# Kernel tuning notes

Measured on AMD Instinct MI355X. Metric: run time of the kernel, lower is better.

Reference implementation:

```python
import jax, jax.numpy as jnp
import numpy as np
from jax import lax

# ---- module config (matches init_kwargs) ----
TARGET_H, TARGET_W = 1024, 1024
SMOOTH_K = 3
DIL_K = 3
DIL_ITERS = 2
DIL_BETA = 5.0
DIL_STRENGTH = 1.0


def _cubic_weights(t):
    """Keys cubic convolution weights (a=-0.75, torch bicubic). t: [N] frac in [0,1). -> [N,4] for taps at offsets -1,0,1,2."""
    a = -0.75
    t1 = t + 1.0  # distance of tap -1
    w0 = a * t1**3 - 5.0 * a * t1**2 + 8.0 * a * t1 - 4.0 * a
    w1 = (a + 2.0) * t**3 - (a + 3.0) * t**2 + 1.0
    u = 1.0 - t
    w2 = (a + 2.0) * u**3 - (a + 3.0) * u**2 + 1.0
    u2 = 2.0 - t
    w3 = a * u2**3 - 5.0 * a * u2**2 + 8.0 * a * u2 - 4.0 * a
    return jnp.stack([w0, w1, w2, w3], axis=-1)


def _taps(n_in, n_out):
    # grid_sample with align_corners=True over a full linspace(-1,1) grid maps
    # output pixel j -> input coord linspace(0, n_in-1, n_out)[j]
    src = jnp.linspace(0.0, n_in - 1.0, n_out)
    i0 = jnp.floor(src)
    t = src - i0
    idx = (i0[:, None] + jnp.arange(-1, 3)[None, :]).astype(jnp.int32)
    idx = jnp.clip(idx, 0, n_in - 1)  # padding_mode='border'
    return idx, _cubic_weights(t)


def _resize_bicubic(x, ht, wt):
    B, C, H, W = x.shape
    ih, wh = _taps(H, ht)
    iw, ww = _taps(W, wt)
    # rows: [B,C,ht,4,W] -> weighted sum over taps
    xr = x[:, :, ih, :]
    xr = jnp.einsum('bcthw,th->bctw', xr.transpose(0, 1, 2, 4, 3), wh) if False else (xr * wh[None, None, :, :, None]).sum(axis=3)
    # cols: [B,C,ht,wt,4]
    xc = xr[:, :, :, iw]
    return (xc * ww[None, None, None, :, :]).sum(axis=-1)


def _gaussian_kernel(k):
    sigma = k / 3.0
    r = np.arange(k, dtype=np.float32) - k // 2
    k1 = np.exp(-0.5 * (r / sigma) ** 2)
    k1 = k1 / k1.sum()
    k2 = np.outer(k1, k1)
    return jnp.asarray(k2.reshape(1, 1, k, k))


def _smooth(x):
    kern = _gaussian_kernel(SMOOTH_K)
    pad = SMOOTH_K // 2
    return lax.conv_general_dilated(
        x, kern, window_strides=(1, 1), padding=[(pad, pad), (pad, pad)],
        dimension_numbers=('NCHW', 'OIHW', 'NCHW'))


def _soft_dilate(x):
    # windowed logsumexp: lse = (1/beta) * log sum_window exp(beta * x),
    # with zero padding inside the window (matches F.unfold padding).
    p = DIL_K // 2
    for _ in range(DIL_ITERS):
        xp = jnp.pad(x, ((0, 0), (0, 0), (p, p), (p, p)))
        e = jnp.exp(DIL_BETA * (xp - 1.0))  # shift by 1.0 (x in [0,1]) for stability
        s = lax.reduce_window(e, 0.0, lax.add, (1, 1, DIL_K, DIL_K), (1, 1, 1, 1), 'VALID')
        x = jnp.clip(1.0 + jnp.log(s) / DIL_BETA, 0.0, 1.0)
    return x  # DIL_STRENGTH == 1.0 -> no blend with original


def setup_inputs() -> dict:
    key = jax.random.key(0)
    detris_output = jax.random.normal(key, (8, 1, 256, 256), dtype=jnp.float32)
    return {"detris_output": detris_output}


def reference(detris_output) -> jnp.ndarray:
    x = jax.nn.sigmoid(detris_output)
    x = _resize_bicubic(x, TARGET_H, TARGET_W)
    x = _smooth(x)
    x = _soft_dilate(x)
    return x
```

## Files before the change

kernel.cpp:

```cpp
#include <hip/hip_runtime.h>
#include <hip/hip_fp16.h>

#define B_ 8
#define HI 256
#define WI 256
#define HO 1024
#define WO 1024

#define TLE 64
#define NRS 24
#define SSTR 25
#define HS 18
#define EW 38
#define SC (255.0f / 1023.0f)
#define F5L2E 7.2134752f
#define EXPM5 0.0067379470f
#define GW0 0.27406862f
#define GW1 0.45186276f
#define C02 0.13862944f

__device__ __forceinline__ int basef(int g) {
    int yc = min(max(g, 0), HO - 1);
    return (int)floorf((float)yc * SC) - 2;
}

__device__ __forceinline__ void tap6(int g, int* base_out, float w[6]) {
    int yc = min(max(g, 0), HO - 1);
    int base = basef(g);
#pragma unroll
    for (int s = 0; s < 6; ++s) w[s] = 0.0f;
    if (g >= 0 && g < HO) {
#pragma unroll
        for (int d = -1; d <= 1; ++d) {
            int yd = yc + d;
            if (yd < 0 || yd >= HO) continue;
            float src = (float)yd * SC;
            float fi0 = floorf(src);
            float tt = src - fi0;
            const float a = -0.75f;
            float t1 = tt + 1.0f;
            float c0 = ((a * t1 - 5.0f * a) * t1 + 8.0f * a) * t1 - 4.0f * a;
            float c1 = ((a + 2.0f) * tt - (a + 3.0f)) * tt * tt + 1.0f;
            float u = 1.0f - tt;
            float c2 = ((a + 2.0f) * u - (a + 3.0f)) * u * u + 1.0f;
            float u2 = 2.0f - tt;
            float c3 = ((a * u2 - 5.0f * a) * u2 + 8.0f * a) * u2 - 4.0f * a;
            int s0 = ((int)fi0 - 1) - base;
            float gg = (d == 0) ? GW1 : GW0;
            w[s0 + 0] += gg * c0;
            w[s0 + 1] += gg * c1;
            w[s0 + 2] += gg * c2;
            w[s0 + 3] += gg * c3;
        }
    }
    *base_out = base;
}

__device__ __forceinline__ void pad8(const float w[6], int d, float scl, float w8[8]) {
#pragma unroll
    for (int j = 0; j < 8; ++j) {
        float a = (j < 6) ? w[j] : 0.0f;
        float bq = (j >= 1 && j < 7) ? w[j - 1] : 0.0f;
        w8[j] = ((d == 0) ? a : bq) * scl;
    }
}

__device__ __forceinline__ uint4 packw8(const float w8[8]) {
    uint4 r;
    r.x = __builtin_bit_cast(unsigned int, __floats2half2_rn(w8[0], w8[1]));
    r.y = __builtin_bit_cast(unsigned int, __floats2half2_rn(w8[2], w8[3]));
    r.z = __builtin_bit_cast(unsigned int, __floats2half2_rn(w8[4], w8[5]));
    r.w = __builtin_bit_cast(unsigned int, __floats2half2_rn(w8[6], w8[7]));
    return r;
}

__device__ __forceinline__ void unpackw8(uint4 p, float w[8]) {
    __half2 a = __builtin_bit_cast(__half2, p.x);
    __half2 bq = __builtin_bit_cast(__half2, p.y);
    __half2 c = __builtin_bit_cast(__half2, p.z);
    __half2 d = __builtin_bit_cast(__half2, p.w);
    w[0] = __low2float(a);  w[1] = __high2float(a);
    w[2] = __low2float(bq); w[3] = __high2float(bq);
    w[4] = __low2float(c);  w[5] = __high2float(c);
    w[6] = __low2float(d);  w[7] = __high2float(d);
}

__global__ __launch_bounds__(256, 8) void k_fused(const float* __restrict__ in,
                                                  float* __restrict__ out) {
    __shared__ __align__(16) unsigned int Eu[68 * EW];
    __shared__ float4 Hs[NRS * HS];
    __shared__ uint4 xWu[72];
    __shared__ uint4 vWu[70];
    __shared__ int vgb[14], xgb[18];
    float* SL = (float*)Eu;

    const int tid = threadIdx.x;
    const int bx = blockIdx.x, by = blockIdx.y, b = blockIdx.z;
    const int gy0 = by * TLE, gx0 = bx * TLE;
    const int rlo = basef(gy0 - 3);
    const int clo = basef(gx0 - 4);

    if (tid < 70) {
        int fy = tid + 1;
        int base; float w[6];
        tap6(gy0 + fy - 3, &base, w);
        int q = tid / 5;
        int bs = basef(gy0 + (1 + 5 * q) - 3);
        float w8[8];
        pad8(w, base - bs, F5L2E, w8);
        vWu[tid] = packw8(w8);
    } else if (tid < 84) {
        vgb[tid - 70] = basef(gy0 + (1 + 5 * (tid - 70)) - 3);
    } else if (tid < 102) {
        xgb[tid - 84] = basef(gx0 + 4 * (tid - 84) - 4);
    } else if (tid >= 128 && tid < 200) {
        int xe = tid - 128;
        int base; float w[6];
        tap6(gx0 + xe - 4, &base, w);
        int bs = basef(gx0 + (xe & ~3) - 4);
        float w8[8];
        pad8(w, base - bs, 1.0f, w8);
        xWu[xe] = packw8(w8);
    }
    {
        const float* pin = in + b * (HI * WI);
        int cc = tid & 31, rr0 = tid >> 5;
        if (cc < NRS) {
            for (int rr = rr0; rr < NRS; rr += 8) {
                int row = min(max(rlo + rr, 0), HI - 1);
                int col = min(max(clo + cc, 0), HI - 1);
                float x = pin[row * WI + col];
                SL[rr * SSTR + cc] = 1.0f / (1.0f + __expf(-x));
            }
        }
    }
    __syncthreads();

    const int ty = tid / HS;
    const int tx = tid - ty * HS;

    if (tid < 252) {
        int cbg = xgb[tx] - clo;
        int wc[8];
#pragma unroll
        for (int j = 0; j < 8; ++j) wc[j] = min(cbg + j, NRS - 1);
        float xw0[8], xw1[8], xw2[8], xw3[8];
        {
            int xe0 = tx << 2;
            unpackw8(xWu[xe0 + 0], xw0);
            unpackw8(xWu[xe0 + 1], xw1);
            unpackw8(xWu[xe0 + 2], xw2);
            unpackw8(xWu[xe0 + 3], xw3);
        }
        for (int r = ty; r < NRS; r += 14) {
            const float* srow = SL + r * SSTR;
            float wnd[8];
#pragma unroll
            for (int j = 0; j < 8; ++j) wnd[j] = srow[wc[j]];
            float s0 = wnd[0]*xw0[0], s1 = wnd[0]*xw1[0], s2 = wnd[0]*xw2[0], s3 = wnd[0]*xw3[0];
#pragma unroll
            for (int j = 1; j < 8; ++j) {
                s0 = fmaf(wnd[j], xw0[j], s0);
                s1 = fmaf(wnd[j], xw1[j], s1);
                s2 = fmaf(wnd[j], xw2[j], s2);
                s3 = fmaf(wnd[j], xw3[j], s3);
            }
            Hs[r * HS + tx] = make_float4(s0, s1, s2, s3);
        }
    }
    __syncthreads();

    if (tid < 252) {
        const int q = ty;
        const int rbase = vgb[q] - rlo;
        float4 h[8];
#pragma unroll
        for (int i = 0; i < 8; ++i) h[i] = Hs[min(rbase + i, NRS - 1) * HS + tx];
#pragma unroll
        for (int i = 0; i < 5; ++i) {
            int fy = 1 + 5 * q + i;
            if (fy <= 68) {
                float wv[8];
                unpackw8(vWu[fy - 1], wv);
                float ax = -F5L2E, ay = -F5L2E, az = -F5L2E, aw = -F5L2E;
#pragma unroll
                for (int j = 0; j < 8; ++j) {
                    ax = fmaf(wv[j], h[j].x, ax);
                    ay = fmaf(wv[j], h[j].y, ay);
                    az = fmaf(wv[j], h[j].z, az);
                    aw = fmaf(wv[j], h[j].w, aw);
                }
                unsigned int p0 = __builtin_bit_cast(unsigned int, __floats2half2_rn(exp2f(ax), exp2f(ay)));
                unsigned int p1 = __builtin_bit_cast(unsigned int, __floats2half2_rn(exp2f(az), exp2f(aw)));
                *reinterpret_cast<uint2*>(&Eu[(fy - 1) * EW + 2 * tx]) = make_uint2(p0, p1);
            }
        }
    }
    __syncthreads();

    {
        const int dx = tid & 15;
        const int sq = tid >> 4;
        const int lr0 = 4 * sq;
        const bool rT = (by == 0)  && (sq == 0);
        const bool rB = (by == 15) && (sq == 15);
        const bool cL = (bx == 0)  && (dx == 0);
        const bool cR = (bx == 15) && (dx == 15);

        auto HSUM = [&](int lr, float hs[6]) {
            unsigned int ua = Eu[lr * EW + 2 * dx + 1];
            uint2 ub = *reinterpret_cast<const uint2*>(&Eu[lr * EW + 2 * dx + 2]);
            unsigned int uc = Eu[lr * EW + 2 * dx + 4];
            __half2 A2 = __builtin_bit_cast(__half2, ua);
            __half2 B2 = __builtin_bit_cast(__half2, ub.x);
            __half2 C2 = __builtin_bit_cast(__half2, ub.y);
            __half2 D2 = __builtin_bit_cast(__half2, uc);
            float e0 = __low2float(A2), e1 = __high2float(A2);
            float e2 = __low2float(B2), e3 = __high2float(B2);
            float e4 = __low2float(C2), e5 = __high2float(C2);
            float e6 = __low2float(D2), e7 = __high2float(D2);
            hs[0] = e0 + e1 + e2;
            hs[1] = e1 + e2 + e3;
            hs[2] = e2 + e3 + e4;
            hs[3] = e3 + e4 + e5;
            hs[4] = e4 + e5 + e6;
            hs[5] = e5 + e6 + e7;
        };
        auto E2F = [&](const float* a, const float* bq, const float* c, bool rowOv) -> float4 {
            float e[6];
#pragma unroll
            for (int j = 0; j < 6; ++j) e[j] = fminf(a[j] + bq[j] + c[j], 1.0f);
            if (rowOv) {
#pragma unroll
                for (int j = 0; j < 6; ++j) e[j] = EXPM5;
            }
            if (cL) e[0] = EXPM5;
            if (cR) e[5] = EXPM5;
            return make_float4(e[0] + e[1] + e[2], e[1] + e[2] + e[3],
                               e[2] + e[3] + e[4], e[3] + e[4] + e[5]);
        };
        auto OUTF = [&](float4 a, float4 bq, float4 c) -> float4 {
            float4 o;
            o.x = fmaxf(fminf(fmaf(C02, __log2f(a.x + bq.x + c.x), 1.0f), 1.0f), 0.0f);
            o.y = fmaxf(fminf(fmaf(C02, __log2f(a.y + bq.y + c.y), 1.0f), 1.0f), 0.0f);
            o.z = fmaxf(fminf(fmaf(C02, __log2f(a.z + bq.z + c.z), 1.0f), 1.0f), 0.0f);
            o.w = fmaxf(fminf(fmaf(C02, __log2f(a.w + bq.w + c.w), 1.0f), 1.0f), 0.0f);
            return o;
        };

        float hA[6], hB[6], hC[6], hD[6];
        size_t obase = ((size_t)(b * HO + by * TLE + 4 * sq) * WO) + bx * TLE + (dx << 2);

        HSUM(lr0 + 0, hA); HSUM(lr0 + 1, hB); HSUM(lr0 + 2, hC);
        float4 eA = E2F(hA, hB, hC, rT);
        HSUM(lr0 + 3, hD); float4 eB = E2F(hB, hC, hD, false);
        HSUM(lr0 + 4, hA); float4 eC = E2F(hC, hD, hA, false);
        *reinterpret_cast<float4*>(out + obase) = OUTF(eA, eB, eC); obase += WO;
        HSUM(lr0 + 5, hB); float4 eD = E2F(hD, hA, hB, false);
        *reinterpret_cast<float4*>(out + obase) = OUTF(eB, eC, eD); obase += WO;
        HSUM(lr0 + 6, hC); float4 eE = E2F(hA, hB, hC, false);
        *reinterpret_cast<float4*>(out + obase) = OUTF(eC, eD, eE); obase += WO;
        HSUM(lr0 + 7, hD); float4 eF = E2F(hB, hC, hD, rB);
        *reinterpret_cast<float4*>(out + obase) = OUTF(eD, eE, eF);
    }
}

extern "C" void kernel_launch(void* const* d_in, const int* in_sizes, int n_in,
                              void* d_out, int out_size, void* d_ws, size_t ws_size,
                              hipStream_t stream) {
    const float* in = (const float*)d_in[0];
    float* out = (float*)d_out;
    dim3 g(WO / TLE, HO / TLE, B_);
    k_fused<<<g, dim3(256), 0, stream>>>(in, out);
}
```

Measured before the change: 24.96 us.

## Give each wavefront its own 32x32 tile to drop block-wide barriers

Restructures the fused kernel so each 64-lane wavefront processes an independent 32x32 output tile with private LDS buffers. This removes all __syncthreads between the sigmoid load, horizontal and vertical bicubic passes, and the dilation stage. The intermediate horizontal-pass results are also stored as fp16 instead of fp32 to cut LDS footprint. The smaller tiles recompute more halo per output and lower fp16 precision in the intermediate, and occupancy hint drops to 7.

```diff
diff --git a/kernel.cpp b/kernel.cpp
--- a/kernel.cpp
+++ b/kernel.cpp
@@ -1,23 +1,18 @@
 #include <hip/hip_runtime.h>
 #include <hip/hip_fp16.h>
 
-#define B_ 8
 #define HI 256
 #define WI 256
 #define HO 1024
 #define WO 1024
-
-#define TLE 64
-#define NRS 24
-#define SSTR 25
-#define HS 18
-#define EW 38
 #define SC (255.0f / 1023.0f)
 #define F5L2E 7.2134752f
 #define EXPM5 0.0067379470f
 #define GW0 0.27406862f
 #define GW1 0.45186276f
 #define C02 0.13862944f
+#define EST 22
+#define SLS 19
 
 __device__ __forceinline__ int basef(int g) {
     int yc = min(max(g, 0), HO - 1);
@@ -59,9 +54,10 @@
 __device__ __forceinline__ void pad8(const float w[6], int d, float scl, float w8[8]) {
 #pragma unroll
     for (int j = 0; j < 8; ++j) {
-        float a = (j < 6) ? w[j] : 0.0f;
-        float bq = (j >= 1 && j < 7) ? w[j - 1] : 0.0f;
-        w8[j] = ((d == 0) ? a : bq) * scl;
+        float v0 = (j < 6) ? w[j] : 0.0f;
+        float v1 = (j >= 1 && j < 7) ? w[j - 1] : 0.0f;
+        float v2 = (j >= 2) ? w[j - 2] : 0.0f;
+        w8[j] = ((d == 0) ? v0 : (d == 1) ? v1 : v2) * scl;
     }
 }
 
@@ -76,88 +72,87 @@
 
 __device__ __forceinline__ void unpackw8(uint4 p, float w[8]) {
     __half2 a = __builtin_bit_cast(__half2, p.x);
-    __half2 bq = __builtin_bit_cast(__half2, p.y);
+    __half2 b = __builtin_bit_cast(__half2, p.y);
     __half2 c = __builtin_bit_cast(__half2, p.z);
     __half2 d = __builtin_bit_cast(__half2, p.w);
     w[0] = __low2float(a);  w[1] = __high2float(a);
-    w[2] = __low2float(bq); w[3] = __high2float(bq);
+    w[2] = __low2float(b);  w[3] = __high2float(b);
     w[4] = __low2float(c);  w[5] = __high2float(c);
     w[6] = __low2float(d);  w[7] = __high2float(d);
 }
 
-__global__ __launch_bounds__(256, 8) void k_fused(const float* __restrict__ in,
+__device__ __forceinline__ void unpack4(uint2 u, float f[4]) {
+    __half2 a = __builtin_bit_cast(__half2, u.x);
+    __half2 b = __builtin_bit_cast(__half2, u.y);
+    f[0] = __low2float(a); f[1] = __high2float(a);
+    f[2] = __low2float(b); f[3] = __high2float(b);
+}
+
+__global__ __launch_bounds__(256, 7) void k_fused(const float* __restrict__ in,
                                                   float* __restrict__ out) {
-    __shared__ __align__(16) unsigned int Eu[68 * EW];
-    __shared__ float4 Hs[NRS * HS];
-    __shared__ uint4 xWu[72];
-    __shared__ uint4 vWu[70];
-    __shared__ int vgb[14], xgb[18];
-    float* SL = (float*)Eu;
+    __shared__ __align__(16) unsigned int Eu[4][36 * EST];
+    __shared__ __align__(16) unsigned int Hu[4][16 * EST];
+    __shared__ uint4 xWu[4][40];
+    __shared__ uint4 vWu[4][36];
 
     const int tid = threadIdx.x;
-    const int bx = blockIdx.x, by = blockIdx.y, b = blockIdx.z;
-    const int gy0 = by * TLE, gx0 = bx * TLE;
-    const int rlo = basef(gy0 - 3);
-    const int clo = basef(gx0 - 4);
-
-    if (tid < 70) {
-        int fy = tid + 1;
-        int base; float w[6];
-        tap6(gy0 + fy - 3, &base, w);
-        int q = tid / 5;
-        int bs = basef(gy0 + (1 + 5 * q) - 3);
+    const int w = tid >> 6, lane = tid & 63;
+    unsigned int* E1 = Eu[w];
+    unsigned int* Hq = Hu[w];
+    uint4* xW = xWu[w];
+    uint4* vW = vWu[w];
+    float* SL = (float*)E1;
+
+    const int tx = (blockIdx.x << 2) + w, ty = blockIdx.y, b = blockIdx.z;
+    const int gx0 = tx << 5, gy0 = ty << 5;
+    const int rlo = basef(gy0 - 2);
+    const int clo = basef(gx0 - 3);
+
+    if (lane < 36) {
+        int base; float w6[6];
+        tap6(gy0 + (lane + 1) - 3, &base, w6);
+        int bs = basef(gy0 + 6 * (lane / 6) - 2);
         float w8[8];
-        pad8(w, base - bs, F5L2E, w8);
-        vWu[tid] = packw8(w8);
-    } else if (tid < 84) {
-        vgb[tid - 70] = basef(gy0 + (1 + 5 * (tid - 70)) - 3);
-    } else if (tid < 102) {
-        xgb[tid - 84] = basef(gx0 + 4 * (tid - 84) - 4);
-    } else if (tid >= 128 && tid < 200) {
-        int xe = tid - 128;
-        int base; float w[6];
-        tap6(gx0 + xe - 4, &base, w);
-        int bs = basef(gx0 + (xe & ~3) - 4);
+        pad8(w6, base - bs, F5L2E, w8);
+        vW[lane] = packw8(w8);
+    }
+    if (lane < 40) {
+        int base; float w6[6];
+        tap6(gx0 + lane - 3, &base, w6);
+        int bs = basef(gx0 + 4 * (lane >> 2) - 3);
         float w8[8];
-        pad8(w, base - bs, 1.0f, w8);
-        xWu[xe] = packw8(w8);
+        pad8(w6, base - bs, 1.0f, w8);
+        xW[lane] = packw8(w8);
     }
     {
         const float* pin = in + b * (HI * WI);
-        int cc = tid & 31, rr0 = tid >> 5;
-        if (cc < NRS) {
-            for (int rr = rr0; rr < NRS; rr += 8) {
-                int row = min(max(rlo + rr, 0), HI - 1);
-                int col = min(max(clo + cc, 0), HI - 1);
-                float x = pin[row * WI + col];
-                SL[rr * SSTR + cc] = 1.0f / (1.0f + __expf(-x));
-            }
-        }
-    }
-    __syncthreads();
-
-    const int ty = tid / HS;
-    const int tx = tid - ty * HS;
-
-    if (tid < 252) {
-        int cbg = xgb[tx] - clo;
-        int wc[8];
-#pragma unroll
-        for (int j = 0; j < 8; ++j) wc[j] = min(cbg + j, NRS - 1);
+        for (int idx = lane; idx < 16 * 18; idx += 64) {
+            int r = idx / 18;
+            int cgi = idx - r * 18;
+            int row = min(max(rlo + r, 0), HI - 1);
+            int col = min(max(clo + cgi, 0), HI - 1);
+            float x = pin[row * WI + col];
+            SL[r * SLS + cgi] = 1.0f / (1.0f + __expf(-x));
+        }
+    }
+
+    const int cg = lane / 10;
+    const int cc = lane - cg * 10;
+
+    if (cg < 6) {
+        int cbg = basef(gx0 + 4 * cc - 3) - clo;
         float xw0[8], xw1[8], xw2[8], xw3[8];
-        {
-            int xe0 = tx << 2;
-            unpackw8(xWu[xe0 + 0], xw0);
-            unpackw8(xWu[xe0 + 1], xw1);
-            unpackw8(xWu[xe0 + 2], xw2);
-            unpackw8(xWu[xe0 + 3], xw3);
-        }
-        for (int r = ty; r < NRS; r += 14) {
-            const float* srow = SL + r * SSTR;
+        unpackw8(xW[4 * cc + 0], xw0);
+        unpackw8(xW[4 * cc + 1], xw1);
+        unpackw8(xW[4 * cc + 2], xw2);
+        unpackw8(xW[4 * cc + 3], xw3);
+        for (int r = cg; r < 16; r += 6) {
+            const float* srow = SL + r * SLS + cbg;
             float wnd[8];
 #pragma unroll
-            for (int j = 0; j < 8; ++j) wnd[j] = srow[wc[j]];
-            float s0 = wnd[0]*xw0[0], s1 = wnd[0]*xw1[0], s2 = wnd[0]*xw2[0], s3 = wnd[0]*xw3[0];
+            for (int j = 0; j < 8; ++j) wnd[j] = srow[j];
+            float s0 = wnd[0] * xw0[0], s1 = wnd[0] * xw1[0];
+            float s2 = wnd[0] * xw2[0], s3 = wnd[0] * xw3[0];
 #pragma unroll
             for (int j = 1; j < 8; ++j) {
                 s0 = fmaf(wnd[j], xw0[j], s0);
@@ -165,66 +160,63 @@
                 s2 = fmaf(wnd[j], xw2[j], s2);
                 s3 = fmaf(wnd[j], xw3[j], s3);
             }
-            Hs[r * HS + tx] = make_float4(s0, s1, s2, s3);
-        }
-    }
-    __syncthreads();
-
-    if (tid < 252) {
-        const int q = ty;
-        const int rbase = vgb[q] - rlo;
-        float4 h[8];
-#pragma unroll
-        for (int i = 0; i < 8; ++i) h[i] = Hs[min(rbase + i, NRS - 1) * HS + tx];
-#pragma unroll
-        for (int i = 0; i < 5; ++i) {
-            int fy = 1 + 5 * q + i;
-            if (fy <= 68) {
-                float wv[8];
-                unpackw8(vWu[fy - 1], wv);
-                float ax = -F5L2E, ay = -F5L2E, az = -F5L2E, aw = -F5L2E;
-#pragma unroll
-                for (int j = 0; j < 8; ++j) {
-                    ax = fmaf(wv[j], h[j].x, ax);
-                    ay = fmaf(wv[j], h[j].y, ay);
-                    az = fmaf(wv[j], h[j].z, az);
-                    aw = fmaf(wv[j], h[j].w, aw);
-                }
-                unsigned int p0 = __builtin_bit_cast(unsigned int, __floats2half2_rn(exp2f(ax), exp2f(ay)));
-                unsigned int p1 = __builtin_bit_cast(unsigned int, __floats2half2_rn(exp2f(az), exp2f(aw)));
-                *reinterpret_cast<uint2*>(&Eu[(fy - 1) * EW + 2 * tx]) = make_uint2(p0, p1);
-            }
-        }
-    }
-    __syncthreads();
+            unsigned int p0 = __builtin_bit_cast(unsigned int, __floats2half2_rn(s0, s1));
+            unsigned int p1 = __builtin_bit_cast(unsigned int, __floats2half2_rn(s2, s3));
+            *reinterpret_cast<uint2*>(&Hq[r * EST + 2 * cc]) = make_uint2(p0, p1);
+        }
+    }
+
+    if (cg < 6) {
+        int rb = basef(gy0 + 6 * cg - 2) - rlo;
+        float hv0[4], hv1[4], hv2[4], hv3[4], hv4[4], hv5[4], hv6[4], hv7[4];
+        unpack4(*reinterpret_cast<const uint2*>(&Hq[(rb + 0) * EST + 2 * cc]), hv0);
+        unpack4(*reinterpret_cast<const uint2*>(&Hq[(rb + 1) * EST + 2 * cc]), hv1);
+        unpack4(*reinterpret_cast<const uint2*>(&Hq[(rb + 2) * EST + 2 * cc]), hv2);
+        unpack4(*reinterpret_cast<const uint2*>(&Hq[(rb + 3) * EST + 2 * cc]), hv3);
+        unpack4(*reinterpret_cast<const uint2*>(&Hq[(rb + 4) * EST + 2 * cc]), hv4);
+        unpack4(*reinterpret_cast<const uint2*>(&Hq[(rb + 5) * EST + 2 * cc]), hv5);
+        unpack4(*reinterpret_cast<const uint2*>(&Hq[(rb + 6) * EST + 2 * cc]), hv6);
+        unpack4(*reinterpret_cast<const uint2*>(&Hq[(rb + 7) * EST + 2 * cc]), hv7);
+#pragma unroll
+        for (int i = 0; i < 6; ++i) {
+            int fy = 1 + 6 * cg + i;
+            float wv[8];
+            unpackw8(vW[fy - 1], wv);
+            float ax = -F5L2E, ay = -F5L2E, az = -F5L2E, aw = -F5L2E;
+#define ACC(H, J) ax = fmaf(wv[J], H[0], ax); ay = fmaf(wv[J], H[1], ay); \
+                  az = fmaf(wv[J], H[2], az); aw = fmaf(wv[J], H[3], aw);
+            ACC(hv0, 0) ACC(hv1, 1) ACC(hv2, 2) ACC(hv3, 3)
+            ACC(hv4, 4) ACC(hv5, 5) ACC(hv6, 6) ACC(hv7, 7)
+#undef ACC
+            unsigned int p0 = __builtin_bit_cast(unsigned int, __floats2half2_rn(exp2f(ax), exp2f(ay)));
+            unsigned int p1 = __builtin_bit_cast(unsigned int, __floats2half2_rn(exp2f(az), exp2f(aw)));
+            *reinterpret_cast<uint2*>(&E1[(fy - 1) * EST + 2 * cc]) = make_uint2(p0, p1);
+        }
+    }
 
     {
-        const int dx = tid & 15;
-        const int sq = tid >> 4;
+        const int dx = lane & 7;
+        const int sq = lane >> 3;
         const int lr0 = 4 * sq;
-        const bool rT = (by == 0)  && (sq == 0);
-        const bool rB = (by == 15) && (sq == 15);
-        const bool cL = (bx == 0)  && (dx == 0);
-        const bool cR = (bx == 15) && (dx == 15);
+        const bool rT = (ty == 0)  && (sq == 0);
+        const bool rB = (ty == 31) && (sq == 7);
+        const bool cL = (tx == 0)  && (dx == 0);
+        const bool cR = (tx == 31) && (dx == 7);
 
         auto HSUM = [&](int lr, float hs[6]) {
-            unsigned int ua = Eu[lr * EW + 2 * dx + 1];
-            uint2 ub = *reinterpret_cast<const uint2*>(&Eu[lr * EW + 2 * dx + 2]);
-            unsigned int uc = Eu[lr * EW + 2 * dx + 4];
-            __half2 A2 = __builtin_bit_cast(__half2, ua);
-            __half2 B2 = __builtin_bit_cast(__half2, ub.x);
-            __half2 C2 = __builtin_bit_cast(__half2, ub.y);
-            __half2 D2 = __builtin_bit_cast(__half2, uc);
-            float e0 = __low2float(A2), e1 = __high2float(A2);
-            float e2 = __low2float(B2), e3 = __high2float(B2);
-            float e4 = __low2float(C2), e5 = __high2float(C2);
-            float e6 = __low2float(D2), e7 = __high2float(D2);
-            hs[0] = e0 + e1 + e2;
-            hs[1] = e1 + e2 + e3;
-            hs[2] = e2 + e3 + e4;
-            hs[3] = e3 + e4 + e5;
-            hs[4] = e4 + e5 + e6;
-            hs[5] = e5 + e6 + e7;
+            uint2 ua = *reinterpret_cast<const uint2*>(&E1[lr * EST + 2 * dx]);
+            uint2 ub = *reinterpret_cast<const uint2*>(&E1[lr * EST + 2 * dx + 2]);
+            unsigned int uc = E1[lr * EST + 2 * dx + 4];
+            float fa[4], fb[4];
+            unpack4(ua, fa); unpack4(ub, fb);
+            __half2 c2 = __builtin_bit_cast(__half2, uc);
+            float f8 = __low2float(c2);
+            hs[0] = fa[1] + fa[2] + fa[3];
+            hs[1] = fa[2] + fa[3] + fb[0];
+            hs[2] = fa[3] + fb[0] + fb[1];
+            hs[3] = fb[0] + fb[1] + fb[2];
+            hs[4] = fb[1] + fb[2] + fb[3];
+            hs[5] = fb[2] + fb[3] + f8;
         };
         auto E2F = [&](const float* a, const float* bq, const float* c, bool rowOv) -> float4 {
             float e[6];
@@ -249,7 +241,7 @@
         };
 
         float hA[6], hB[6], hC[6], hD[6];
-        size_t obase = ((size_t)(b * HO + by * TLE + 4 * sq) * WO) + bx * TLE + (dx << 2);
+        size_t obase = ((size_t)(b * HO + gy0 + 4 * sq) * WO) + gx0 + (dx << 2);
 
         HSUM(lr0 + 0, hA); HSUM(lr0 + 1, hB); HSUM(lr0 + 2, hC);
         float4 eA = E2F(hA, hB, hC, rT);
@@ -270,6 +262,6 @@
                               hipStream_t stream) {
     const float* in = (const float*)d_in[0];
     float* out = (float*)d_out;
-    dim3 g(WO / TLE, HO / TLE, B_);
+    dim3 g(8, 32, 8);
     k_fused<<<g, dim3(256), 0, stream>>>(in, out);
 }
```

Result: slower. 28.07 us (+12.5%).
